# Optimization experiments

Hardware: AMD Instinct MI355X
Metric: run time of the kernel (lower is better)

The kernel has to match this reference:

```python
import jax, jax.numpy as jnp
import numpy as np

NUM_HEAD = 8
DIM_MODEL = 512
DIM_HEAD = DIM_MODEL // NUM_HEAD
LN_EPS = 1e-5


def setup_inputs() -> dict:
    key = jax.random.key(0)
    ks = jax.random.split(key, 12)
    B, L, D = 4, 2048, DIM_MODEL
    s = 0.02
    return {
        "x": jax.random.normal(ks[0], (B, L, D), dtype=jnp.float32),
        "Wq": jax.random.normal(ks[1], (D, D), dtype=jnp.float32) * s,
        "bq": jnp.zeros((D,), dtype=jnp.float32),
        "Wk": jax.random.normal(ks[2], (D, D), dtype=jnp.float32) * s,
        "bk": jnp.zeros((D,), dtype=jnp.float32),
        "Wv": jax.random.normal(ks[3], (D, D), dtype=jnp.float32) * s,
        "bv": jnp.zeros((D,), dtype=jnp.float32),
        "Wo": jax.random.normal(ks[4], (D, D), dtype=jnp.float32) * s,
        "bo": jnp.zeros((D,), dtype=jnp.float32),
        "gamma": jnp.ones((D,), dtype=jnp.float32),
        "beta": jnp.zeros((D,), dtype=jnp.float32),
    }


def reference(x, Wq, bq, Wk, bk, Wv, bv, Wo, bo, gamma, beta):
    B, L, D = x.shape
    H, dh = NUM_HEAD, D // NUM_HEAD
    # QKV projections (torch Linear: x @ W.T + b)
    Q = x @ Wq.T + bq
    K = x @ Wk.T + bk
    V = x @ Wv.T + bv
    # Faithful to the torch code: contiguous view(B*H, L, dh)
    Q = Q.reshape(B * H, L, dh)
    K = K.reshape(B * H, L, dh)
    V = V.reshape(B * H, L, dh)
    scale = dh ** (-0.5)
    # [B*H, L, L] scores, scaled, softmax over keys
    attn = jax.nn.softmax(jnp.einsum("bqd,bkd->bqk", Q, K) * scale, axis=-1)
    context = jnp.einsum("bqk,bkd->bqd", attn, V)  # [B*H, L, dh]
    context = context.reshape(B, L, D)
    out = context @ Wo.T + bo
    out = out + x  # residual (dropout p=0.0 -> identity)
    # LayerNorm over last dim
    mu = jnp.mean(out, axis=-1, keepdims=True)
    var = jnp.mean(jnp.square(out - mu), axis=-1, keepdims=True)
    out = (out - mu) / jnp.sqrt(var + LN_EPS) * gamma + beta
    return out
```

## Files before the change

### kernel.cpp

```cpp
#include <hip/hip_runtime.h>

typedef __bf16 bf16;
typedef __bf16 bf16x4 __attribute__((ext_vector_type(4)));
typedef __bf16 bf16x8 __attribute__((ext_vector_type(8)));
typedef float f32x4 __attribute__((ext_vector_type(4)));

#define MFMA16(A, B, C) __builtin_amdgcn_mfma_f32_16x16x32_bf16((A), (B), (C), 0, 0, 0)

constexpr int Dm   = 512;
constexpr int Lm   = 2048;
constexpr int DH   = 64;
constexpr int Mrows = 8192;
constexpr int NHEADS = 32;

__device__ __forceinline__ void gload16(const void* g, void* l) {
    __builtin_amdgcn_global_load_lds(
        (const __attribute__((address_space(1))) void*)g,
        (__attribute__((address_space(3))) void*)l, 16, 0, 0);
}

__global__ __launch_bounds__(256)
void cvt_kernel(const float* __restrict__ x, const float* __restrict__ Wq,
                const float* __restrict__ Wk, const float* __restrict__ Wv,
                const float* __restrict__ Wo,
                bf16* __restrict__ xb, bf16* __restrict__ Wqb, bf16* __restrict__ Wkb,
                bf16* __restrict__ Wvb, bf16* __restrict__ Wob)
{
    size_t i = ((size_t)blockIdx.x * 256 + threadIdx.x) * 4;
    const float* src; bf16* dst; size_t off;
    if (i < (size_t)Mrows * Dm) {
        src = x; dst = xb; off = i;
    } else {
        size_t r = i - (size_t)Mrows * Dm;
        int w = (int)(r >> 18);
        off = r & 262143;
        src = (w == 0) ? Wq : (w == 1) ? Wk : (w == 2) ? Wv : Wo;
        dst = (w == 0) ? Wqb : (w == 1) ? Wkb : (w == 2) ? Wvb : Wob;
    }
    float4 v = *reinterpret_cast<const float4*>(src + off);
    bf16x4 o; o[0] = (bf16)v.x; o[1] = (bf16)v.y; o[2] = (bf16)v.z; o[3] = (bf16)v.w;
    *reinterpret_cast<bf16x4*>(dst + off) = o;
}

__global__ __launch_bounds__(256)
void qkv_gemm(const bf16* __restrict__ xb,
              const bf16* __restrict__ Wqb, const float* __restrict__ bq,
              const bf16* __restrict__ Wkb, const float* __restrict__ bk,
              const bf16* __restrict__ Wvb, const float* __restrict__ bv,
              bf16* __restrict__ Qo, bf16* __restrict__ Ko, bf16* __restrict__ Vo)
{
    __shared__ bf16 Asm[128 * 64];
    __shared__ bf16 Bsm[128 * 64];

    const int z = blockIdx.z;
    const bf16* W = (z == 0) ? Wqb : (z == 1) ? Wkb : Wvb;
    const float* bias = (z == 0) ? bq : (z == 1) ? bk : bv;
    bf16* out = (z == 0) ? Qo : (z == 1) ? Ko : Vo;

    const int tid = threadIdx.x;
    const int row0 = blockIdx.y * 128;
    const int col0 = blockIdx.x * 128;

    const int wv = tid >> 6;
    const int ln = tid & 63;
    const int wr = wv >> 1, wc = wv & 1;
    const int lr = ln & 15;
    const int lg = ln >> 4;

    const int srow_b = wv * 8 + (ln >> 3);
    const int ssc = ((ln & 7) ^ (ln >> 3)) * 8;

    f32x4 acc[4][4] = {};

    for (int kt = 0; kt < Dm; kt += 64) {
        __syncthreads();
        #pragma unroll
        for (int j = 0; j < 4; ++j) {
            const int row = j * 32 + srow_b;
            const int base = (j * 256 + wv * 64) * 8;
            gload16(xb + (size_t)(row0 + row) * Dm + kt + ssc, &Asm[base]);
            gload16(W + (size_t)(col0 + row) * Dm + kt + ssc, &Bsm[base]);
        }
        __syncthreads();

        #pragma unroll
        for (int ks = 0; ks < 2; ++ks) {
            bf16x8 af[4], bfv[4];
            #pragma unroll
            for (int m = 0; m < 4; ++m) {
                const int R = wr * 64 + m * 16 + lr;
                af[m] = *reinterpret_cast<const bf16x8*>(&Asm[R * 64 + (((ks * 4 + lg) ^ (R & 7)) * 8)]);
            }
            #pragma unroll
            for (int n = 0; n < 4; ++n) {
                const int R = wc * 64 + n * 16 + lr;
                bfv[n] = *reinterpret_cast<const bf16x8*>(&Bsm[R * 64 + (((ks * 4 + lg) ^ (R & 7)) * 8)]);
            }
            #pragma unroll
            for (int m = 0; m < 4; ++m)
                #pragma unroll
                for (int n = 0; n < 4; ++n)
                    acc[m][n] = MFMA16(af[m], bfv[n], acc[m][n]);
        }
    }

    #pragma unroll
    for (int m = 0; m < 4; ++m)
        #pragma unroll
        for (int n = 0; n < 4; ++n)
            #pragma unroll
            for (int i = 0; i < 4; ++i) {
                int r = row0 + wr * 64 + m * 16 + lg * 4 + i;
                int c = col0 + wc * 64 + n * 16 + lr;
                out[(size_t)r * Dm + c] = (bf16)(acc[m][n][i] + bias[c]);
            }
}

__global__ __launch_bounds__(256)
void oproj_gemm(const bf16* __restrict__ ctx, const bf16* __restrict__ Wob,
                const float* __restrict__ bo, const float* __restrict__ x,
                float* __restrict__ tmp)
{
    __shared__ bf16 Asm[128 * 64];
    __shared__ bf16 Bsm[128 * 64];

    const int tid = threadIdx.x;
    const int row0 = blockIdx.y * 128;
    const int col0 = blockIdx.x * 128;

    const int wv = tid >> 6;
    const int ln = tid & 63;
    const int wr = wv >> 1, wc = wv & 1;
    const int lr = ln & 15;
    const int lg = ln >> 4;

    const int srow_b = wv * 8 + (ln >> 3);
    const int ssc = ((ln & 7) ^ (ln >> 3)) * 8;

    f32x4 acc[4][4] = {};

    for (int kt = 0; kt < Dm; kt += 64) {
        __syncthreads();
        #pragma unroll
        for (int j = 0; j < 4; ++j) {
            const int row = j * 32 + srow_b;
            const int base = (j * 256 + wv * 64) * 8;
            gload16(ctx + (size_t)(row0 + row) * Dm + kt + ssc, &Asm[base]);
            gload16(Wob + (size_t)(col0 + row) * Dm + kt + ssc, &Bsm[base]);
        }
        __syncthreads();

        #pragma unroll
        for (int ks = 0; ks < 2; ++ks) {
            bf16x8 af[4], bfv[4];
            #pragma unroll
            for (int m = 0; m < 4; ++m) {
                const int R = wr * 64 + m * 16 + lr;
                af[m] = *reinterpret_cast<const bf16x8*>(&Asm[R * 64 + (((ks * 4 + lg) ^ (R & 7)) * 8)]);
            }
            #pragma unroll
            for (int n = 0; n < 4; ++n) {
                const int R = wc * 64 + n * 16 + lr;
                bfv[n] = *reinterpret_cast<const bf16x8*>(&Bsm[R * 64 + (((ks * 4 + lg) ^ (R & 7)) * 8)]);
            }
            #pragma unroll
            for (int m = 0; m < 4; ++m)
                #pragma unroll
                for (int n = 0; n < 4; ++n)
                    acc[m][n] = MFMA16(af[m], bfv[n], acc[m][n]);
        }
    }

    #pragma unroll
    for (int m = 0; m < 4; ++m)
        #pragma unroll
        for (int n = 0; n < 4; ++n)
            #pragma unroll
            for (int i = 0; i < 4; ++i) {
                int r = row0 + wr * 64 + m * 16 + lg * 4 + i;
                int c = col0 + wc * 64 + n * 16 + lr;
                tmp[(size_t)r * Dm + c] = acc[m][n][i] + bo[c] + x[(size_t)r * Dm + c];
            }
}

__global__ __launch_bounds__(256)
void vt_kernel(const bf16* __restrict__ V, bf16* __restrict__ Vt)
{
    __shared__ bf16 T[64 * 72];
    const int head = blockIdx.y;
    const int k0 = blockIdx.x * 64;
    const size_t hb = (size_t)head * (Lm * DH);
    const int tid = threadIdx.x;
    const int r = tid >> 2;
    const int seg = (tid & 3) * 16;

    {
        const bf16* src = &V[hb + (size_t)(k0 + r) * DH + seg];
        *reinterpret_cast<bf16x8*>(&T[r * 72 + seg])     = reinterpret_cast<const bf16x8*>(src)[0];
        *reinterpret_cast<bf16x8*>(&T[r * 72 + seg + 8]) = reinterpret_cast<const bf16x8*>(src)[1];
    }
    __syncthreads();
    bf16 o[16];
    #pragma unroll
    for (int j = 0; j < 16; ++j) o[j] = T[(seg + j) * 72 + r];
    *reinterpret_cast<bf16x8*>(&Vt[hb + (size_t)r * Lm + k0 + seg])     = *reinterpret_cast<bf16x8*>(&o[0]);
    *reinterpret_cast<bf16x8*>(&Vt[hb + (size_t)r * Lm + k0 + seg + 8]) = *reinterpret_cast<bf16x8*>(&o[8]);
}

__global__ __launch_bounds__(512)
void flash_attn(const bf16* __restrict__ Q, const bf16* __restrict__ K,
                const bf16* __restrict__ Vt, bf16* __restrict__ ctx)
{
    __shared__ bf16 Ksm[2][64 * 76];
    __shared__ bf16 Vsm[2][64 * 76];
    __shared__ bf16 Psm[128 * 76];

    const int head = blockIdx.y;
    const int q0 = blockIdx.x * 128;
    const size_t hb = (size_t)head * (Lm * DH);

    const int tid = threadIdx.x;
    const int wv = tid >> 6;
    const int ln = tid & 63;
    const int lr = ln & 15;
    const int lg = ln >> 4;

    const int srow = tid >> 3;
    const int sseg = (tid & 7) * 8;
    const int sb = srow * 76 + sseg;

    const float qscale = 0.125f * 1.44269504088896340736f;
    bf16x8 qf[2];
    {
        const int qrow = q0 + wv * 16 + lr;
        #pragma unroll
        for (int s = 0; s < 2; ++s) {
            bf16x8 t = *reinterpret_cast<const bf16x8*>(&Q[hb + (size_t)qrow * DH + s * 32 + lg * 8]);
            #pragma unroll
            for (int j = 0; j < 8; ++j) qf[s][j] = (bf16)((float)t[j] * qscale);
        }
    }

    f32x4 cfr[4] = {};
    float lsum[4] = {};

    const bf16* Kp = &K[hb + (size_t)srow * DH + sseg];
    const bf16* Vp = &Vt[hb + (size_t)srow * Lm + sseg];

    bf16x8 kreg = *reinterpret_cast<const bf16x8*>(Kp);
    bf16x8 vreg = *reinterpret_cast<const bf16x8*>(Vp);
    *reinterpret_cast<bf16x8*>(&Ksm[0][sb]) = kreg;
    *reinterpret_cast<bf16x8*>(&Vsm[0][sb]) = vreg;
    kreg = *reinterpret_cast<const bf16x8*>(Kp + 64 * DH);
    vreg = *reinterpret_cast<const bf16x8*>(Vp + 64);
    __syncthreads();

    constexpr int NT = Lm / 64;
    for (int t = 0; t < NT; ++t) {
        const int cur = t & 1;
        if (t + 1 < NT) {
            *reinterpret_cast<bf16x8*>(&Ksm[cur ^ 1][sb]) = kreg;
            *reinterpret_cast<bf16x8*>(&Vsm[cur ^ 1][sb]) = vreg;
        }
        if (t + 2 < NT) {
            kreg = *reinterpret_cast<const bf16x8*>(Kp + (size_t)(t + 2) * 64 * DH);
            vreg = *reinterpret_cast<const bf16x8*>(Vp + (t + 2) * 64);
        }

        f32x4 sfr[4] = {};
        __builtin_amdgcn_s_setprio(1);
        #pragma unroll
        for (int s = 0; s < 2; ++s)
            #pragma unroll
            for (int g = 0; g < 4; ++g) {
                bf16x8 kf = *reinterpret_cast<const bf16x8*>(&Ksm[cur][(g * 16 + lr) * 76 + s * 32 + lg * 8]);
                sfr[g] = MFMA16(qf[s], kf, sfr[g]);
            }
        __builtin_amdgcn_s_setprio(0);

        #pragma unroll
        for (int g = 0; g < 4; ++g)
            #pragma unroll
            for (int i = 0; i < 4; ++i) {
                float p = exp2f(sfr[g][i]);
                lsum[i] += p;
                Psm[(wv * 16 + lg * 4 + i) * 76 + g * 16 + lr] = (bf16)p;
            }

        __builtin_amdgcn_s_setprio(1);
        #pragma unroll
        for (int s = 0; s < 2; ++s) {
            bf16x8 pa = *reinterpret_cast<const bf16x8*>(&Psm[(wv * 16 + lr) * 76 + s * 32 + lg * 8]);
            #pragma unroll
            for (int n = 0; n < 4; ++n) {
                bf16x8 vb = *reinterpret_cast<const bf16x8*>(&Vsm[cur][(n * 16 + lr) * 76 + s * 32 + lg * 8]);
                cfr[n] = MFMA16(pa, vb, cfr[n]);
            }
        }
        __builtin_amdgcn_s_setprio(0);

        __syncthreads();
    }

    #pragma unroll
    for (int off = 1; off < 16; off <<= 1)
        #pragma unroll
        for (int i = 0; i < 4; ++i) lsum[i] += __shfl_xor(lsum[i], off);

    float inv[4];
    #pragma unroll
    for (int i = 0; i < 4; ++i) inv[i] = 1.f / lsum[i];
    #pragma unroll
    for (int n = 0; n < 4; ++n)
        #pragma unroll
        for (int i = 0; i < 4; ++i) {
            int q = q0 + wv * 16 + lg * 4 + i;
            int d = n * 16 + lr;
            ctx[hb + (size_t)q * DH + d] = (bf16)(cfr[n][i] * inv[i]);
        }
}

__global__ __launch_bounds__(128)
void ln_kernel(const float* __restrict__ tmp, const float* __restrict__ gamma,
               const float* __restrict__ beta, float* __restrict__ out)
{
    const int row = blockIdx.x;
    const int tid = threadIdx.x;
    const int wv = tid >> 6;
    const int ln = tid & 63;

    float4 v = reinterpret_cast<const float4*>(tmp + (size_t)row * Dm)[tid];
    float s = v.x + v.y + v.z + v.w;
    float sq = v.x * v.x + v.y * v.y + v.z * v.z + v.w * v.w;

    #pragma unroll
    for (int off = 32; off > 0; off >>= 1) {
        s += __shfl_down(s, off);
        sq += __shfl_down(sq, off);
    }
    __shared__ float red[4];
    if (ln == 0) { red[wv * 2] = s; red[wv * 2 + 1] = sq; }
    __syncthreads();
    s = red[0] + red[2];
    sq = red[1] + red[3];

    const float mu = s * (1.f / Dm);
    const float var = sq * (1.f / Dm) - mu * mu;
    const float rstd = rsqrtf(var + 1e-5f);

    float4 g = reinterpret_cast<const float4*>(gamma)[tid];
    float4 b = reinterpret_cast<const float4*>(beta)[tid];
    float4 o;
    o.x = (v.x - mu) * rstd * g.x + b.x;
    o.y = (v.y - mu) * rstd * g.y + b.y;
    o.z = (v.z - mu) * rstd * g.z + b.z;
    o.w = (v.w - mu) * rstd * g.w + b.w;
    reinterpret_cast<float4*>(out + (size_t)row * Dm)[tid] = o;
}

extern "C" void kernel_launch(void* const* d_in, const int* in_sizes, int n_in,
                              void* d_out, int out_size, void* d_ws, size_t ws_size,
                              hipStream_t stream)
{
    const float* x  = (const float*)d_in[0];
    const float* Wq = (const float*)d_in[1];
    const float* bq = (const float*)d_in[2];
    const float* Wk = (const float*)d_in[3];
    const float* bk = (const float*)d_in[4];
    const float* Wv = (const float*)d_in[5];
    const float* bv = (const float*)d_in[6];
    const float* Wo = (const float*)d_in[7];
    const float* bo = (const float*)d_in[8];
    const float* gamma = (const float*)d_in[9];
    const float* beta  = (const float*)d_in[10];
    float* out = (float*)d_out;

    const size_t MD = (size_t)Mrows * Dm;
    const size_t WD = (size_t)Dm * Dm;
    char* p = (char*)d_ws;
    bf16* xb  = (bf16*)p;                 p += MD * 2;
    bf16* Qw  = (bf16*)p;                 p += MD * 2;
    bf16* Kw  = (bf16*)p;                 p += MD * 2;
    bf16* Vw  = (bf16*)p;                 p += MD * 2;
    bf16* Vtw = (bf16*)p;                 p += MD * 2;
    bf16* Wqb = (bf16*)p;                 p += WD * 2;
    bf16* Wkb = (bf16*)p;                 p += WD * 2;
    bf16* Wvb = (bf16*)p;                 p += WD * 2;
    bf16* Wob = (bf16*)p;                 p += WD * 2;
    float* Tw = (float*)d_ws;
    bf16* Cw = Vw;

    {
        const size_t total = MD + 4 * WD;
        cvt_kernel<<<dim3((unsigned)(total / (256 * 4))), 256, 0, stream>>>(
            x, Wq, Wk, Wv, Wo, xb, Wqb, Wkb, Wvb, Wob);
    }

    qkv_gemm<<<dim3(Dm / 128, Mrows / 128, 3), 256, 0, stream>>>(
        xb, Wqb, bq, Wkb, bk, Wvb, bv, Qw, Kw, Vw);

    vt_kernel<<<dim3(Lm / 64, NHEADS), 256, 0, stream>>>(Vw, Vtw);

    flash_attn<<<dim3(Lm / 128, NHEADS), 512, 0, stream>>>(Qw, Kw, Vtw, Cw);

    oproj_gemm<<<dim3(Dm / 128, Mrows / 128), 256, 0, stream>>>(Cw, Wob, bo, x, Tw);

    ln_kernel<<<dim3(Mrows), 128, 0, stream>>>(Tw, gamma, beta, out);
}
```

Baseline: 203.7 us.

## Switch flash attention to 32x32 MFMA with register-resident P fragments

The attention kernel moves from 16x16x32 MFMA to 32x32x16 MFMA, computing S^T = K·Q^T so each lane holds probabilities for one query column. P is repacked into the B-operand layout with lane shuffles instead of going through shared memory, which removes the Psm buffer and its LDS round trip. Each block now covers 256 queries (32 per wave), doubling K/V tile reuse and halving the grid. The cost is more register pressure from the 16-wide accumulators, shuffle overhead, and fewer blocks to spread across the CUs.

```diff
diff --git a/kernel.cpp b/kernel.cpp
--- a/kernel.cpp
+++ b/kernel.cpp
@@ -4,8 +4,11 @@
 typedef __bf16 bf16x4 __attribute__((ext_vector_type(4)));
 typedef __bf16 bf16x8 __attribute__((ext_vector_type(8)));
 typedef float f32x4 __attribute__((ext_vector_type(4)));
+typedef float f32x16 __attribute__((ext_vector_type(16)));
+typedef unsigned int u32;
 
 #define MFMA16(A, B, C) __builtin_amdgcn_mfma_f32_16x16x32_bf16((A), (B), (C), 0, 0, 0)
+#define MFMA32(A, B, C) __builtin_amdgcn_mfma_f32_32x32x16_bf16((A), (B), (C), 0, 0, 0)
 
 constexpr int Dm   = 512;
 constexpr int Lm   = 2048;
@@ -17,6 +20,12 @@
     __builtin_amdgcn_global_load_lds(
         (const __attribute__((address_space(1))) void*)g,
         (__attribute__((address_space(3))) void*)l, 16, 0, 0);
+}
+
+__device__ __forceinline__ u32 pack2(float a, float b) {
+    unsigned short la = __builtin_bit_cast(unsigned short, (bf16)a);
+    unsigned short lb = __builtin_bit_cast(unsigned short, (bf16)b);
+    return (u32)la | ((u32)lb << 16);
 }
 
 __global__ __launch_bounds__(256)
@@ -213,39 +222,38 @@
 {
     __shared__ bf16 Ksm[2][64 * 76];
     __shared__ bf16 Vsm[2][64 * 76];
-    __shared__ bf16 Psm[128 * 76];
 
     const int head = blockIdx.y;
-    const int q0 = blockIdx.x * 128;
+    const int q0 = blockIdx.x * 256;
     const size_t hb = (size_t)head * (Lm * DH);
 
     const int tid = threadIdx.x;
     const int wv = tid >> 6;
     const int ln = tid & 63;
-    const int lr = ln & 15;
-    const int lg = ln >> 4;
+    const int q31 = ln & 31;
+    const int hi = ln >> 5;
 
     const int srow = tid >> 3;
-    const int sseg = (tid & 7) * 8;
-    const int sb = srow * 76 + sseg;
+    const int scu  = tid & 7;
+    const int sb = srow * 76 + scu * 8;
+
+    const int qrow = q0 + wv * 32 + q31;
 
     const float qscale = 0.125f * 1.44269504088896340736f;
-    bf16x8 qf[2];
-    {
-        const int qrow = q0 + wv * 16 + lr;
-        #pragma unroll
-        for (int s = 0; s < 2; ++s) {
-            bf16x8 t = *reinterpret_cast<const bf16x8*>(&Q[hb + (size_t)qrow * DH + s * 32 + lg * 8]);
-            #pragma unroll
-            for (int j = 0; j < 8; ++j) qf[s][j] = (bf16)((float)t[j] * qscale);
-        }
-    }
-
-    f32x4 cfr[4] = {};
-    float lsum[4] = {};
-
-    const bf16* Kp = &K[hb + (size_t)srow * DH + sseg];
-    const bf16* Vp = &Vt[hb + (size_t)srow * Lm + sseg];
+    bf16x8 qf[4];
+    #pragma unroll
+    for (int c = 0; c < 4; ++c) {
+        bf16x8 t = *reinterpret_cast<const bf16x8*>(&Q[hb + (size_t)qrow * DH + c * 16 + hi * 8]);
+        #pragma unroll
+        for (int j = 0; j < 8; ++j) qf[c][j] = (bf16)((float)t[j] * qscale);
+    }
+
+    f32x16 acc0 = {};
+    f32x16 acc1 = {};
+    float lsum = 0.f;
+
+    const bf16* Kp = &K[hb + (size_t)srow * DH + scu * 8];
+    const bf16* Vp = &Vt[hb + (size_t)srow * Lm + scu * 8];
 
     bf16x8 kreg = *reinterpret_cast<const bf16x8*>(Kp);
     bf16x8 vreg = *reinterpret_cast<const bf16x8*>(Vp);
@@ -267,57 +275,74 @@
             vreg = *reinterpret_cast<const bf16x8*>(Vp + (t + 2) * 64);
         }
 
-        f32x4 sfr[4] = {};
-        __builtin_amdgcn_s_setprio(1);
-        #pragma unroll
-        for (int s = 0; s < 2; ++s)
-            #pragma unroll
-            for (int g = 0; g < 4; ++g) {
-                bf16x8 kf = *reinterpret_cast<const bf16x8*>(&Ksm[cur][(g * 16 + lr) * 76 + s * 32 + lg * 8]);
-                sfr[g] = MFMA16(qf[s], kf, sfr[g]);
-            }
-        __builtin_amdgcn_s_setprio(0);
-
-        #pragma unroll
-        for (int g = 0; g < 4; ++g)
-            #pragma unroll
-            for (int i = 0; i < 4; ++i) {
-                float p = exp2f(sfr[g][i]);
-                lsum[i] += p;
-                Psm[(wv * 16 + lg * 4 + i) * 76 + g * 16 + lr] = (bf16)p;
-            }
-
-        __builtin_amdgcn_s_setprio(1);
-        #pragma unroll
-        for (int s = 0; s < 2; ++s) {
-            bf16x8 pa = *reinterpret_cast<const bf16x8*>(&Psm[(wv * 16 + lr) * 76 + s * 32 + lg * 8]);
-            #pragma unroll
-            for (int n = 0; n < 4; ++n) {
-                bf16x8 vb = *reinterpret_cast<const bf16x8*>(&Vsm[cur][(n * 16 + lr) * 76 + s * 32 + lg * 8]);
-                cfr[n] = MFMA16(pa, vb, cfr[n]);
-            }
-        }
-        __builtin_amdgcn_s_setprio(0);
+        #pragma unroll
+        for (int kb = 0; kb < 2; ++kb) {
+            f32x16 s = {};
+            __builtin_amdgcn_s_setprio(1);
+            #pragma unroll
+            for (int c = 0; c < 4; ++c) {
+                bf16x8 kf = *reinterpret_cast<const bf16x8*>(
+                    &Ksm[cur][(kb * 32 + q31) * 76 + (c * 2 + hi) * 8]);
+                s = MFMA32(kf, qf[c], s);
+            }
+            __builtin_amdgcn_s_setprio(0);
+
+            float p[16];
+            #pragma unroll
+            for (int r = 0; r < 16; ++r) { p[r] = exp2f(s[r]); lsum += p[r]; }
+
+            u32 pk_[8], xk[8];
+            #pragma unroll
+            for (int r = 0; r < 8; ++r) pk_[r] = pack2(p[2 * r], p[2 * r + 1]);
+            #pragma unroll
+            for (int r = 0; r < 8; ++r) xk[r] = (u32)__shfl_xor((int)pk_[r], 32);
+
+            union PFrag { u32 w[4]; bf16x8 v; } f0, f1;
+            f0.w[0] = hi ? xk[2] : pk_[0];
+            f0.w[1] = hi ? xk[3] : pk_[1];
+            f0.w[2] = hi ? pk_[2] : xk[0];
+            f0.w[3] = hi ? pk_[3] : xk[1];
+            f1.w[0] = hi ? xk[6] : pk_[4];
+            f1.w[1] = hi ? xk[7] : pk_[5];
+            f1.w[2] = hi ? pk_[6] : xk[4];
+            f1.w[3] = hi ? pk_[7] : xk[5];
+
+            __builtin_amdgcn_s_setprio(1);
+            {
+                bf16x8 v00 = *reinterpret_cast<const bf16x8*>(
+                    &Vsm[cur][(q31) * 76 + (kb * 4 + hi) * 8]);
+                acc0 = MFMA32(v00, f0.v, acc0);
+                bf16x8 v01 = *reinterpret_cast<const bf16x8*>(
+                    &Vsm[cur][(q31) * 76 + (kb * 4 + 2 + hi) * 8]);
+                acc0 = MFMA32(v01, f1.v, acc0);
+                bf16x8 v10 = *reinterpret_cast<const bf16x8*>(
+                    &Vsm[cur][(32 + q31) * 76 + (kb * 4 + hi) * 8]);
+                acc1 = MFMA32(v10, f0.v, acc1);
+                bf16x8 v11 = *reinterpret_cast<const bf16x8*>(
+                    &Vsm[cur][(32 + q31) * 76 + (kb * 4 + 2 + hi) * 8]);
+                acc1 = MFMA32(v11, f1.v, acc1);
+            }
+            __builtin_amdgcn_s_setprio(0);
+        }
 
         __syncthreads();
     }
 
-    #pragma unroll
-    for (int off = 1; off < 16; off <<= 1)
-        #pragma unroll
-        for (int i = 0; i < 4; ++i) lsum[i] += __shfl_xor(lsum[i], off);
-
-    float inv[4];
-    #pragma unroll
-    for (int i = 0; i < 4; ++i) inv[i] = 1.f / lsum[i];
-    #pragma unroll
-    for (int n = 0; n < 4; ++n)
+    lsum += __shfl_xor(lsum, 32);
+    const float inv = 1.f / lsum;
+
+    #pragma unroll
+    for (int g8 = 0; g8 < 4; ++g8) {
+        bf16x4 o0, o1;
         #pragma unroll
         for (int i = 0; i < 4; ++i) {
-            int q = q0 + wv * 16 + lg * 4 + i;
-            int d = n * 16 + lr;
-            ctx[hb + (size_t)q * DH + d] = (bf16)(cfr[n][i] * inv[i]);
-        }
+            o0[i] = (bf16)(acc0[g8 * 4 + i] * inv);
+            o1[i] = (bf16)(acc1[g8 * 4 + i] * inv);
+        }
+        const int d0 = g8 * 8 + hi * 4;
+        *reinterpret_cast<bf16x4*>(&ctx[hb + (size_t)qrow * DH + d0])      = o0;
+        *reinterpret_cast<bf16x4*>(&ctx[hb + (size_t)qrow * DH + 32 + d0]) = o1;
+    }
 }
 
 __global__ __launch_bounds__(128)
@@ -401,7 +426,7 @@
 
     vt_kernel<<<dim3(Lm / 64, NHEADS), 256, 0, stream>>>(Vw, Vtw);
 
-    flash_attn<<<dim3(Lm / 128, NHEADS), 512, 0, stream>>>(Qw, Kw, Vtw, Cw);
+    flash_attn<<<dim3(Lm / 256, NHEADS), 512, 0, stream>>>(Qw, Kw, Vtw, Cw);
 
     oproj_gemm<<<dim3(Dm / 128, Mrows / 128), 256, 0, stream>>>(Cw, Wob, bo, x, Tw);
 
```

After: 202.0 us. No clear change (-0.8%).
